# Performance work log

Measured on AMD Instinct MI355X. Metric: run time of the kernel, lower is better.

## Reference

```python
import jax, jax.numpy as jnp
import numpy as np

B, T, D, W, H = 64, 512, 768, 255, 8
DH = D // H

def layernorm(x, g, b, eps=1e-5):
    m = jnp.mean(x, axis=-1, keepdims=True)
    v = jnp.mean((x - m) ** 2, axis=-1, keepdims=True)
    return (x - m) * jax.lax.rsqrt(v + eps) * g + b

def setup_inputs() -> dict:
    key = jax.random.key(0)
    ks = list(jax.random.split(key, 12))
    p = lambda k, shape, s=0.02: (jax.random.normal(k, shape, jnp.float32) * s)
    # words_ids: -100 at CLS/SEP, each word spans 2 subtokens -> 255 words/row
    wi = np.full((B, T), -100, dtype=np.int32)
    pos = np.arange(1, T - 1)
    wi[:, 1:T - 1] = (pos - 1) // 2
    return {
        'output_bert': jax.random.normal(ks[0], (B, T, D), jnp.float32),
        'words_ids': jnp.asarray(wi),
        'Wq': p(ks[1], (D, D)), 'bq': jnp.zeros((D,), jnp.float32),
        'Wk': p(ks[2], (D, D)), 'bk': jnp.zeros((D,), jnp.float32),
        'Wv': p(ks[3], (D, D)), 'bv': jnp.zeros((D,), jnp.float32),
        'Wo': p(ks[4], (D, D)), 'bo': jnp.zeros((D,), jnp.float32),
        'ln1_g': jnp.ones((D,), jnp.float32), 'ln1_b': jnp.zeros((D,), jnp.float32),
        'W1f': p(ks[5], (D, 4 * D)), 'b1f': jnp.zeros((4 * D,), jnp.float32),
        'W2f': p(ks[6], (4 * D, D)), 'b2f': jnp.zeros((D,), jnp.float32),
        'ln2_g': jnp.ones((D,), jnp.float32), 'ln2_b': jnp.zeros((D,), jnp.float32),
        'ng': jnp.ones((D,), jnp.float32), 'nb': jnp.zeros((D,), jnp.float32),
        'lin_w': p(ks[7], (D, 2)), 'lin_b': jnp.zeros((2,), jnp.float32),
    }

def reference(output_bert, words_ids, Wq, bq, Wk, bk, Wv, bv, Wo, bo,
              ln1_g, ln1_b, W1f, b1f, W2f, b2f, ln2_g, ln2_b, ng, nb, lin_w, lin_b):
    Bsz = output_bert.shape[0]
    # --- first-subtoken gather: first token position of each word id ---
    hits = words_ids[:, None, :] == jnp.arange(W)[None, :, None]   # [B, W, T]
    first_idx = jnp.argmax(hits, axis=-1)                           # [B, W]
    feat = jnp.take_along_axis(output_bert, first_idx[..., None], axis=1)  # [B, W, D]
    # --- transformer encoder layer (post-norm, relu FFN) ---
    q = (feat @ Wq + bq).reshape(Bsz, W, H, DH)
    k = (feat @ Wk + bk).reshape(Bsz, W, H, DH)
    v = (feat @ Wv + bv).reshape(Bsz, W, H, DH)
    scores = jnp.einsum('bqhd,bkhd->bhqk', q, k) * (1.0 / np.sqrt(DH))
    attn = jax.nn.softmax(scores, axis=-1)
    ctx = jnp.einsum('bhqk,bkhd->bqhd', attn, v).reshape(Bsz, W, D)
    x = layernorm(feat + ctx @ Wo + bo, ln1_g, ln1_b)
    ff = jax.nn.relu(x @ W1f + b1f) @ W2f + b2f
    x = layernorm(x + ff, ln2_g, ln2_b)
    # --- final LayerNorm + Linear + softmax + argmax path ---
    x = layernorm(x, ng, nb)
    logits = x @ lin_w + lin_b
    ner_prob = jax.nn.softmax(logits, axis=-1)
    path = jnp.argmax(ner_prob, axis=-1)
    return ner_prob, path
```

## Files before the change

kernel.cpp:

```cpp
#include <hip/hip_runtime.h>
#include <cmath>

#define Bsz 64
#define Tt  512
#define Dd  768
#define Wn  255
#define Hh  8
#define DHd 96
#define NROWS (Bsz*Wn)

typedef _Float16 half_t;
typedef _Float16 f16x8 __attribute__((ext_vector_type(8)));
typedef _Float16 f16x4 __attribute__((ext_vector_type(4)));
typedef float f32x4 __attribute__((ext_vector_type(4)));

#define OFF_QKV_H 0
#define OFF_QKV_L 1769472
#define OFF_WO_H 3538944
#define OFF_WO_L 4128768
#define OFF_W1_H 4718592
#define OFF_W1_L 7077888
#define OFF_W2_H 9437184
#define OFF_W2_L 11796480
#define SLOTH 25165824
__device__ __align__(16) half_t g_w16[14155776];

__device__ __forceinline__ void gload16(const half_t* g, half_t* l) {
    __builtin_amdgcn_global_load_lds((const __attribute__((address_space(1))) void*)g,
                                     (__attribute__((address_space(3))) void*)l, 16, 0, 0);
}


__global__ void k_init_fi(int* fi) {
    int i = blockIdx.x * 256 + threadIdx.x;
    if (i < Bsz * Wn) fi[i] = 0x7fffffff;
}

__global__ void k_scan(const int* __restrict__ wid, int* __restrict__ fi) {
    int i = blockIdx.x * 256 + threadIdx.x;
    if (i >= Bsz * Tt) return;
    int b = i / Tt, t = i % Tt;
    int w = wid[i];
    if (w >= 0 && w < Wn) atomicMin(&fi[b * Wn + w], t);
}

__global__ void k_bcat(const float* __restrict__ bq, const float* __restrict__ bk,
                       const float* __restrict__ bv, float* __restrict__ o) {
    int i = blockIdx.x * 256 + threadIdx.x;
    if (i < 768) o[i] = bq[i];
    else if (i < 1536) o[i] = bk[i - 768];
    else if (i < 2304) o[i] = bv[i - 1536];
}

__global__ void k_gather(const float4* __restrict__ ob, const int* __restrict__ fi,
                         half_t* __restrict__ f16) {
    int i = blockIdx.x * 256 + threadIdx.x;
    if (i >= NROWS * 192) return;
    int r = i / 192, c = i % 192;
    int b = r / Wn;
    int idx = fi[r];
    if (idx == 0x7fffffff) idx = 0;
    float4 v = ob[((size_t)b * Tt + idx) * 192 + c];
    float a0 = v.x * 16.f, a1 = v.y * 16.f, a2 = v.z * 16.f, a3 = v.w * 16.f;
    half_t h0 = (half_t)a0, h1 = (half_t)a1, h2 = (half_t)a2, h3 = (half_t)a3;
    f16x4 hv = {h0, h1, h2, h3};
    f16x4 lv = {(half_t)(a0 - (float)h0), (half_t)(a1 - (float)h1),
                (half_t)(a2 - (float)h2), (half_t)(a3 - (float)h3)};
    size_t off = (size_t)r * 1536 + c * 4;
    *(f16x4*)&f16[off] = hv;
    *(f16x4*)&f16[off + 768] = lv;
}


__global__ void k_wsplit(const float* __restrict__ Wm, int K, int N,
                         size_t off_h, size_t off_l) {
    __shared__ float sm[32][33];
    const int tx = threadIdx.x, ty = threadIdx.y;
    const int n0 = blockIdx.x * 32, k0 = blockIdx.y * 32;
    #pragma unroll
    for (int r = 0; r < 4; ++r)
        sm[ty + r * 8][tx] = Wm[(size_t)(k0 + ty + r * 8) * N + n0 + tx];
    __syncthreads();
    half_t* oh = g_w16 + off_h;
    half_t* ol = g_w16 + off_l;
    #pragma unroll
    for (int r = 0; r < 4; ++r) {
        float v = 64.f * sm[tx][ty + r * 8];
        half_t hi = (half_t)v;
        size_t o = (size_t)(n0 + ty + r * 8) * K + k0 + tx;
        oh[o] = hi;
        ol[o] = (half_t)(v - (float)hi);
    }
}


template<int MODE, int AMODE, int NTILE>
__global__ __launch_bounds__(256, NTILE == 64 ? 3 : 2) void k_gemm16(
    const half_t* __restrict__ Ah, const half_t* __restrict__ Al, int lda,
    size_t boff_h, size_t boff_l,
    const float* __restrict__ bias,
    const void* __restrict__ res,
    void* __restrict__ out0, void* __restrict__ out1,
    int M, int N, int K) {
    constexpr int MI = (NTILE == 128 ? 4 : 2);
    __shared__ half_t sA[2][128 * 32];
    __shared__ half_t sB[2][NTILE * 32];
    const int tid = threadIdx.x;
    const int w = tid >> 6, l = tid & 63;
    int lin = blockIdx.y * gridDim.x + blockIdx.x;
    int rpx = gridDim.y >> 3;
    int j_ = lin >> 3;
    int jr = j_ / gridDim.x;
    int by = (lin & 7) * rpx + jr;
    int bx = j_ - jr * gridDim.x;
    const int row0 = by * 128, col0 = bx * NTILE;
    const half_t* Bh = g_w16 + boff_h;
    const half_t* Bl = g_w16 + boff_l;

    const int srow = l >> 2;
    const int skk  = (l & 3) * 8;
    const int fr = l & 15, qk = (l >> 4) * 8;
    const int mh = (NTILE == 128) ? (w >> 1) * 64 : w * 32;
    const int nh = (NTILE == 128) ? (w & 1) * 64 : 0;

    f32x4 acc[MI][4];
    #pragma unroll
    for (int i = 0; i < MI; ++i)
        #pragma unroll
        for (int j = 0; j < 4; ++j) acc[i][j] = (f32x4){0.f, 0.f, 0.f, 0.f};

    for (int k0 = 0; k0 < K; k0 += 32) {
        #pragma unroll
        for (int t = 0; t < 2; ++t) {
            int r = (w * 2 + t) * 16 + srow;
            int grA = row0 + r; if (grA >= M) grA = M - 1;
            half_t* da  = (half_t*)&sA[0][(w * 2 + t) * 512];
            half_t* da2 = (half_t*)&sA[1][(w * 2 + t) * 512];
            if (AMODE == 1) {
                int b = grA / 255, wl = grA - b * 255;
                int kk = k0 + skk;
                int h = kk / 96, d = kk - h * 96;
                size_t aoff = ((size_t)(b * 8 + h) * 256 + wl) * 192 + d;
                gload16(Ah + aoff, da);
                gload16(Al + aoff, da2);
            } else {
                gload16(Ah + (size_t)grA * lda + k0 + skk, da);
                gload16(Al + (size_t)grA * lda + k0 + skk, da2);
            }
            if (NTILE == 128 || t == 0) {
                int bs = (NTILE == 128) ? (w * 2 + t) : w;
                int grB = col0 + bs * 16 + srow;
                gload16(Bh + (size_t)grB * K + k0 + skk, (half_t*)&sB[0][bs * 512]);
                gload16(Bl + (size_t)grB * K + k0 + skk, (half_t*)&sB[1][bs * 512]);
            }
        }
        __syncthreads();
        f16x8 a0[MI], a1[MI], b0[4], b1[4];
        #pragma unroll
        for (int i = 0; i < MI; ++i) {
            a0[i] = *(const f16x8*)&sA[0][(mh + i * 16 + fr) * 32 + qk];
            a1[i] = *(const f16x8*)&sA[1][(mh + i * 16 + fr) * 32 + qk];
        }
        #pragma unroll
        for (int j = 0; j < 4; ++j) {
            b0[j] = *(const f16x8*)&sB[0][(nh + j * 16 + fr) * 32 + qk];
            b1[j] = *(const f16x8*)&sB[1][(nh + j * 16 + fr) * 32 + qk];
        }
        #pragma unroll
        for (int i = 0; i < MI; ++i)
            #pragma unroll
            for (int j = 0; j < 4; ++j) {
                acc[i][j] = __builtin_amdgcn_mfma_f32_16x16x32_f16(a0[i], b0[j], acc[i][j], 0, 0, 0);
                acc[i][j] = __builtin_amdgcn_mfma_f32_16x16x32_f16(a0[i], b1[j], acc[i][j], 0, 0, 0);
                acc[i][j] = __builtin_amdgcn_mfma_f32_16x16x32_f16(a1[i], b0[j], acc[i][j], 0, 0, 0);
            }
        __syncthreads();
    }

    const float dsc = 1.0f / 1024.0f;
    #pragma unroll
    for (int i = 0; i < MI; ++i) {
        #pragma unroll
        for (int r = 0; r < 4; ++r) {
            int row = row0 + mh + i * 16 + ((l >> 4) << 2) + r;
            if (row >= M) continue;
            #pragma unroll
            for (int j = 0; j < 4; ++j) {
                int col = col0 + nh + j * 16 + (l & 15);
                float vv = acc[i][j][r] * dsc + bias[col];
                if (MODE == 5) {
                    int b = row / 255, wl = row - b * 255;
                    int part = col / 768;
                    int cc = col - part * 768;
                    int h = cc / 96, d = cc - h * 96;
                    float t16 = vv * 16.f;
                    half_t hi = (half_t)t16;
                    half_t lo = (half_t)(t16 - (float)hi);
                    half_t* dst = (half_t*)out0 + (size_t)part * SLOTH;
                    size_t o = ((size_t)(b * 8 + h) * 256 + wl) * 192 + d;
                    dst[o] = hi; dst[o + 96] = lo;
                } else if (MODE == 1) {
                    const half_t* rp = (const half_t*)res;
                    vv += ((float)rp[(size_t)row * 1536 + col] +
                           (float)rp[(size_t)row * 1536 + 768 + col]) * 0.0625f;
                    ((float*)out0)[(size_t)row * N + col] = vv;
                } else if (MODE == 2) {
                    vv = fmaxf(vv, 0.f);
                    float t16 = vv * 16.f;
                    half_t hi = (half_t)t16;
                    ((half_t*)out0)[(size_t)row * N + col] = hi;
                    ((half_t*)out1)[(size_t)row * N + col] = (half_t)(t16 - (float)hi);
                } else {
                    vv += ((const float*)res)[(size_t)row * N + col];
                    ((float*)out0)[(size_t)row * N + col] = vv;
                }
            }
        }
    }
}


__global__ __launch_bounds__(256, 2) void k_attn2(half_t* __restrict__ qc,
                                                  const half_t* __restrict__ kk16,
                                                  const half_t* __restrict__ vv16) {
    __shared__ half_t sK[64][200];
    __shared__ half_t sVT[192][72];
    __shared__ float  sP[4][16][68];
    const int tid = threadIdx.x;
    const int w = tid >> 6, l = tid & 63;
    const int lr = l & 15, lc = l >> 4;
    const size_t base = (size_t)blockIdx.x * 49152;
    const float ssc = 0.10206207261596575f / 256.0f;

    for (int pass = 0; pass < 2; ++pass) {
        f32x4 O[2][6];
        float mrow[2][4], lrow[2][4];
        #pragma unroll
        for (int qs = 0; qs < 2; ++qs) {
            #pragma unroll
            for (int dn = 0; dn < 6; ++dn) O[qs][dn] = (f32x4){0.f, 0.f, 0.f, 0.f};
            #pragma unroll
            for (int r = 0; r < 4; ++r) { mrow[qs][r] = -3e38f; lrow[qs][r] = 0.f; }
        }
        for (int kt = 0; kt < 4; ++kt) {
            __syncthreads();
            #pragma unroll
            for (int c = 0; c < 6; ++c) {
                int ch = w + c * 4;
                *(f16x8*)&sK[l][ch * 8] =
                    *(const f16x8*)(kk16 + base + (size_t)(kt * 64 + l) * 192 + ch * 8);
            }
            #pragma unroll
            for (int c = 0; c < 6; ++c) {
                int ch = w + c * 4;
                f16x8 vv = *(const f16x8*)(vv16 + base + (size_t)(kt * 64 + l) * 192 + ch * 8);
                #pragma unroll
                for (int j = 0; j < 8; ++j) sVT[ch * 8 + j][l] = vv[j];
            }
            __syncthreads();
            #pragma unroll
            for (int qs = 0; qs < 2; ++qs) {
                const int qrow0 = (pass * 2 + qs) * 64 + w * 16;
                f16x8 qf0[3], qf1[3];
                #pragma unroll
                for (int s = 0; s < 3; ++s) {
                    qf0[s] = *(const f16x8*)(qc + base + (size_t)(qrow0 + lr) * 192 + s * 32 + lc * 8);
                    qf1[s] = *(const f16x8*)(qc + base + (size_t)(qrow0 + lr) * 192 + 96 + s * 32 + lc * 8);
                }
                f32x4 sacc[4];
                #pragma unroll
                for (int nt = 0; nt < 4; ++nt) sacc[nt] = (f32x4){0.f, 0.f, 0.f, 0.f};
                #pragma unroll
                for (int s = 0; s < 3; ++s)
                    #pragma unroll
                    for (int nt = 0; nt < 4; ++nt) {
                        f16x8 kh = *(const f16x8*)&sK[nt * 16 + lr][s * 32 + lc * 8];
                        f16x8 klo = *(const f16x8*)&sK[nt * 16 + lr][96 + s * 32 + lc * 8];
                        sacc[nt] = __builtin_amdgcn_mfma_f32_16x16x32_f16(qf0[s], kh, sacc[nt], 0, 0, 0);
                        sacc[nt] = __builtin_amdgcn_mfma_f32_16x16x32_f16(qf0[s], klo, sacc[nt], 0, 0, 0);
                        sacc[nt] = __builtin_amdgcn_mfma_f32_16x16x32_f16(qf1[s], kh, sacc[nt], 0, 0, 0);
                    }
                float sv[4][4], mx[4] = {-3e38f, -3e38f, -3e38f, -3e38f};
                #pragma unroll
                for (int nt = 0; nt < 4; ++nt) {
                    int key = kt * 64 + nt * 16 + lr;
                    #pragma unroll
                    for (int r = 0; r < 4; ++r) {
                        float s_ = sacc[nt][r] * ssc;
                        if (key >= 255) s_ = -3e38f;
                        sv[nt][r] = s_;
                        mx[r] = fmaxf(mx[r], s_);
                    }
                }
                #pragma unroll
                for (int r = 0; r < 4; ++r) {
                    mx[r] = fmaxf(mx[r], __shfl_xor(mx[r], 1));
                    mx[r] = fmaxf(mx[r], __shfl_xor(mx[r], 2));
                    mx[r] = fmaxf(mx[r], __shfl_xor(mx[r], 4));
                    mx[r] = fmaxf(mx[r], __shfl_xor(mx[r], 8));
                }
                float alpha[4], rsum[4];
                #pragma unroll
                for (int r = 0; r < 4; ++r) {
                    float mn = fmaxf(mrow[qs][r], mx[r]);
                    alpha[r] = __expf(mrow[qs][r] - mn);
                    mrow[qs][r] = mn;
                    rsum[r] = 0.f;
                }
                float pv[4][4];
                #pragma unroll
                for (int nt = 0; nt < 4; ++nt)
                    #pragma unroll
                    for (int r = 0; r < 4; ++r) {
                        float p = __expf(sv[nt][r] - mrow[qs][r]);
                        pv[nt][r] = p;
                        rsum[r] += p;
                    }
                #pragma unroll
                for (int r = 0; r < 4; ++r) {
                    rsum[r] += __shfl_xor(rsum[r], 1);
                    rsum[r] += __shfl_xor(rsum[r], 2);
                    rsum[r] += __shfl_xor(rsum[r], 4);
                    rsum[r] += __shfl_xor(rsum[r], 8);
                    lrow[qs][r] = lrow[qs][r] * alpha[r] + rsum[r];
                }
                #pragma unroll
                for (int dn = 0; dn < 6; ++dn)
                    #pragma unroll
                    for (int r = 0; r < 4; ++r) O[qs][dn][r] *= alpha[r];
                #pragma unroll
                for (int nt = 0; nt < 4; ++nt)
                    #pragma unroll
                    for (int r = 0; r < 4; ++r)
                        sP[w][lc * 4 + r][nt * 16 + lr] = pv[nt][r];
                #pragma unroll
                for (int ks = 0; ks < 2; ++ks) {
                    const float* pp = &sP[w][lr][ks * 32 + lc * 8];
                    f16x8 ph, pl;
                    #pragma unroll
                    for (int j = 0; j < 8; ++j) {
                        float p = pp[j];
                        half_t h_ = (half_t)p;
                        ph[j] = h_;
                        pl[j] = (half_t)(p - (float)h_);
                    }
                    #pragma unroll
                    for (int dn = 0; dn < 6; ++dn) {
                        f16x8 vh = *(const f16x8*)&sVT[dn * 16 + lr][ks * 32 + lc * 8];
                        f16x8 vl = *(const f16x8*)&sVT[96 + dn * 16 + lr][ks * 32 + lc * 8];
                        O[qs][dn] = __builtin_amdgcn_mfma_f32_16x16x32_f16(ph, vh, O[qs][dn], 0, 0, 0);
                        O[qs][dn] = __builtin_amdgcn_mfma_f32_16x16x32_f16(ph, vl, O[qs][dn], 0, 0, 0);
                        O[qs][dn] = __builtin_amdgcn_mfma_f32_16x16x32_f16(pl, vh, O[qs][dn], 0, 0, 0);
                    }
                }
            }
        }
        #pragma unroll
        for (int qs = 0; qs < 2; ++qs) {
            const int qrow0 = (pass * 2 + qs) * 64 + w * 16;
            #pragma unroll
            for (int r = 0; r < 4; ++r) {
                int qrow = qrow0 + lc * 4 + r;
                if (qrow >= Wn) continue;
                float inv = 1.0f / lrow[qs][r];
                #pragma unroll
                for (int dn = 0; dn < 6; ++dn) {
                    float val = O[qs][dn][r] * inv;
                    half_t hi = (half_t)val;
                    half_t lo = (half_t)(val - (float)hi);
                    size_t o = base + (size_t)qrow * 192 + dn * 16 + lr;
                    qc[o] = hi;
                    qc[o + 96] = lo;
                }
            }
        }
    }
}


__global__ __launch_bounds__(256) void k_ln1(const float* __restrict__ X, const float* __restrict__ g,
                                             const float* __restrict__ bt, float* __restrict__ Y,
                                             half_t* __restrict__ Y16) {
    const int r = blockIdx.x, tid = threadIdx.x;
    __shared__ float red[256];
    const float* x = X + (size_t)r * Dd;
    float x0 = x[tid], x1 = x[tid + 256], x2 = x[tid + 512];
    red[tid] = x0 + x1 + x2; __syncthreads();
    for (int s = 128; s > 0; s >>= 1) { if (tid < s) red[tid] += red[tid + s]; __syncthreads(); }
    float mean = red[0] * (1.0f / 768.0f);
    __syncthreads();
    float d0 = x0 - mean, d1 = x1 - mean, d2 = x2 - mean;
    red[tid] = d0 * d0 + d1 * d1 + d2 * d2; __syncthreads();
    for (int s = 128; s > 0; s >>= 1) { if (tid < s) red[tid] += red[tid + s]; __syncthreads(); }
    float rs = rsqrtf(red[0] * (1.0f / 768.0f) + 1e-5f);
    float* y = Y + (size_t)r * Dd;
    float y0 = d0 * rs * g[tid]       + bt[tid];
    float y1 = d1 * rs * g[tid + 256] + bt[tid + 256];
    float y2 = d2 * rs * g[tid + 512] + bt[tid + 512];
    y[tid] = y0; y[tid + 256] = y1; y[tid + 512] = y2;
    half_t* h = Y16 + (size_t)r * 1536;
    float t0 = y0 * 16.f, t1 = y1 * 16.f, t2 = y2 * 16.f;
    half_t h0 = (half_t)t0, h1 = (half_t)t1, h2 = (half_t)t2;
    h[tid] = h0; h[tid + 256] = h1; h[tid + 512] = h2;
    h[768 + tid] = (half_t)(t0 - (float)h0);
    h[768 + tid + 256] = (half_t)(t1 - (float)h1);
    h[768 + tid + 512] = (half_t)(t2 - (float)h2);
}


__global__ __launch_bounds__(256) void k_final2(const float* __restrict__ X,
                                                const float* __restrict__ g2, const float* __restrict__ b2,
                                                const float* __restrict__ ng, const float* __restrict__ nb,
                                                const float* __restrict__ lw, const float* __restrict__ lb,
                                                float* __restrict__ out) {
    const int r = blockIdx.x, tid = threadIdx.x;
    __shared__ float red[256];
    const float* x = X + (size_t)r * Dd;
    float x0 = x[tid], x1 = x[tid + 256], x2 = x[tid + 512];
    red[tid] = x0 + x1 + x2; __syncthreads();
    for (int s = 128; s > 0; s >>= 1) { if (tid < s) red[tid] += red[tid + s]; __syncthreads(); }
    float mean = red[0] * (1.0f / 768.0f);
    __syncthreads();
    float d0 = x0 - mean, d1 = x1 - mean, d2 = x2 - mean;
    red[tid] = d0 * d0 + d1 * d1 + d2 * d2; __syncthreads();
    for (int s = 128; s > 0; s >>= 1) { if (tid < s) red[tid] += red[tid + s]; __syncthreads(); }
    float rs = rsqrtf(red[0] * (1.0f / 768.0f) + 1e-5f);
    __syncthreads();
    float y0 = d0 * rs * g2[tid]       + b2[tid];
    float y1 = d1 * rs * g2[tid + 256] + b2[tid + 256];
    float y2 = d2 * rs * g2[tid + 512] + b2[tid + 512];
    red[tid] = y0 + y1 + y2; __syncthreads();
    for (int s = 128; s > 0; s >>= 1) { if (tid < s) red[tid] += red[tid + s]; __syncthreads(); }
    mean = red[0] * (1.0f / 768.0f);
    __syncthreads();
    float e0 = y0 - mean, e1 = y1 - mean, e2 = y2 - mean;
    red[tid] = e0 * e0 + e1 * e1 + e2 * e2; __syncthreads();
    for (int s = 128; s > 0; s >>= 1) { if (tid < s) red[tid] += red[tid + s]; __syncthreads(); }
    rs = rsqrtf(red[0] * (1.0f / 768.0f) + 1e-5f);
    __syncthreads();
    float n0 = e0 * rs * ng[tid]       + nb[tid];
    float n1 = e1 * rs * ng[tid + 256] + nb[tid + 256];
    float n2 = e2 * rs * ng[tid + 512] + nb[tid + 512];
    float l0 = n0 * lw[2 * tid]     + n1 * lw[2 * (tid + 256)]     + n2 * lw[2 * (tid + 512)];
    float l1 = n0 * lw[2 * tid + 1] + n1 * lw[2 * (tid + 256) + 1] + n2 * lw[2 * (tid + 512) + 1];
    red[tid] = l0; __syncthreads();
    for (int s = 128; s > 0; s >>= 1) { if (tid < s) red[tid] += red[tid + s]; __syncthreads(); }
    l0 = red[0]; __syncthreads();
    red[tid] = l1; __syncthreads();
    for (int s = 128; s > 0; s >>= 1) { if (tid < s) red[tid] += red[tid + s]; __syncthreads(); }
    l1 = red[0];
    if (tid == 0) {
        l0 += lb[0]; l1 += lb[1];
        float m = fmaxf(l0, l1);
        float e0_ = expf(l0 - m), e1_ = expf(l1 - m);
        float inv = 1.0f / (e0_ + e1_);
        out[2 * r] = e0_ * inv;
        out[2 * r + 1] = e1_ * inv;
        out[2 * NROWS + r] = (l1 > l0) ? 1.0f : 0.0f;
    }
}


extern "C" void kernel_launch(void* const* d_in, const int* in_sizes, int n_in,
                              void* d_out, int out_size, void* d_ws, size_t ws_size,
                              hipStream_t stream) {
    const float* ob  = (const float*)d_in[0];
    const int*   wid = (const int*)d_in[1];
    const float* Wq  = (const float*)d_in[2];  const float* bq  = (const float*)d_in[3];
    const float* Wk  = (const float*)d_in[4];  const float* bk  = (const float*)d_in[5];
    const float* Wv  = (const float*)d_in[6];  const float* bv  = (const float*)d_in[7];
    const float* Wo  = (const float*)d_in[8];  const float* bo  = (const float*)d_in[9];
    const float* g1  = (const float*)d_in[10]; const float* b1  = (const float*)d_in[11];
    const float* W1f = (const float*)d_in[12]; const float* b1f = (const float*)d_in[13];
    const float* W2f = (const float*)d_in[14]; const float* b2f = (const float*)d_in[15];
    const float* g2  = (const float*)d_in[16]; const float* b2  = (const float*)d_in[17];
    const float* ng  = (const float*)d_in[18]; const float* nb  = (const float*)d_in[19];
    const float* lw  = (const float*)d_in[20]; const float* lb  = (const float*)d_in[21];
    float* out = (float*)d_out;

    char* ws = (char*)d_ws;
    const size_t MB = 1u << 20;
    const size_t SLOT = 48 * MB;
    int* fi = (int*)ws;
    float* bcat = (float*)(ws + 262144);
    char* S1 = ws + MB;
    char* S2 = S1 + SLOT;
    char* S3 = S2 + SLOT;
    char* S4 = S3 + SLOT;

    half_t* feat16 = (half_t*)S1;
    half_t* q16    = (half_t*)S2;
    half_t* k16    = (half_t*)S3;
    half_t* v16    = (half_t*)S4;
    float*  t1     = (float*)S3;
    float*  xbuf   = (float*)S4;
    half_t* x16    = (half_t*)S2;
    half_t* ffh_h  = (half_t*)S1;
    half_t* ffh_l  = (half_t*)S3;
    float*  t2     = (float*)S2;

    k_wsplit<<<dim3(24, 24), dim3(32, 8), 0, stream>>>(Wq, 768, 768, 0, 1769472);
    k_wsplit<<<dim3(24, 24), dim3(32, 8), 0, stream>>>(Wk, 768, 768, 589824, 2359296);
    k_wsplit<<<dim3(24, 24), dim3(32, 8), 0, stream>>>(Wv, 768, 768, 1179648, 2949120);
    k_wsplit<<<dim3(24, 24), dim3(32, 8), 0, stream>>>(Wo, 768, 768, OFF_WO_H, OFF_WO_L);
    k_wsplit<<<dim3(96, 24), dim3(32, 8), 0, stream>>>(W1f, 768, 3072, OFF_W1_H, OFF_W1_L);
    k_wsplit<<<dim3(24, 96), dim3(32, 8), 0, stream>>>(W2f, 3072, 768, OFF_W2_H, OFF_W2_L);
    k_bcat<<<9, 256, 0, stream>>>(bq, bk, bv, bcat);

    k_init_fi<<<(Bsz * Wn + 255) / 256, 256, 0, stream>>>(fi);
    k_scan<<<(Bsz * Tt) / 256, 256, 0, stream>>>(wid, fi);
    k_gather<<<(NROWS * 192 + 255) / 256, 256, 0, stream>>>((const float4*)ob, fi, feat16);

    k_gemm16<5, 0, 128><<<dim3(18, 128), 256, 0, stream>>>(
        feat16, feat16 + 768, 1536, OFF_QKV_H, OFF_QKV_L,
        bcat, nullptr, q16, nullptr, NROWS, 2304, Dd);

    k_attn2<<<Bsz * Hh, 256, 0, stream>>>(q16, k16, v16);

    k_gemm16<1, 1, 128><<<dim3(6, 128), 256, 0, stream>>>(
        q16, q16 + 96, 0, OFF_WO_H, OFF_WO_L,
        bo, feat16, t1, nullptr, NROWS, Dd, Dd);
    k_ln1<<<NROWS, 256, 0, stream>>>(t1, g1, b1, xbuf, x16);

    for (int c = 0; c < 2; ++c) {
        const int r0 = c * 8160, mc = 8160;
        k_gemm16<2, 0, 128><<<dim3(24, 64), 256, 0, stream>>>(
            x16 + (size_t)r0 * 1536, x16 + (size_t)r0 * 1536 + 768, 1536,
            OFF_W1_H, OFF_W1_L, b1f, nullptr, ffh_h, ffh_l, mc, 3072, Dd);
        k_gemm16<3, 0, 64><<<dim3(12, 64), 256, 0, stream>>>(
            ffh_h, ffh_l, 3072, OFF_W2_H, OFF_W2_L, b2f, xbuf + (size_t)r0 * Dd,
            t2 + (size_t)r0 * Dd, nullptr, mc, Dd, 3072);
    }

    k_final2<<<NROWS, 256, 0, stream>>>(t2, g2, b2, ng, nb, lw, lb, out);
}
```

Before: 1.256 ms.

## Split attention blocks across query quarters with smaller key tiles for occupancy

The attention kernel now launches one block per (batch, head, 64-query chunk) instead of one block per (batch, head) looping over two passes. Key tiles shrink from 64 to 32 keys, which cuts shared memory and allows four blocks per CU. This raises parallelism and occupancy, at the cost of reloading K and V once per query chunk.

New measurement: 1.314 ms. 4.6% more time.

```diff
diff --git a/kernel.cpp b/kernel.cpp
--- a/kernel.cpp
+++ b/kernel.cpp
@@ -220,159 +220,148 @@
 }
 
 
-__global__ __launch_bounds__(256, 2) void k_attn2(half_t* __restrict__ qc,
+__global__ __launch_bounds__(256, 4) void k_attn3(half_t* __restrict__ qc,
                                                   const half_t* __restrict__ kk16,
                                                   const half_t* __restrict__ vv16) {
-    __shared__ half_t sK[64][200];
-    __shared__ half_t sVT[192][72];
-    __shared__ float  sP[4][16][68];
+    __shared__ half_t sK[32][200];
+    __shared__ half_t sVT[192][40];
+    __shared__ float  sP[4][16][36];
     const int tid = threadIdx.x;
     const int w = tid >> 6, l = tid & 63;
     const int lr = l & 15, lc = l >> 4;
-    const size_t base = (size_t)blockIdx.x * 49152;
+    const int bh = blockIdx.x >> 2, qq = blockIdx.x & 3;
+    const size_t base = (size_t)bh * 49152;
     const float ssc = 0.10206207261596575f / 256.0f;
-
-    for (int pass = 0; pass < 2; ++pass) {
-        f32x4 O[2][6];
-        float mrow[2][4], lrow[2][4];
-        #pragma unroll
-        for (int qs = 0; qs < 2; ++qs) {
-            #pragma unroll
-            for (int dn = 0; dn < 6; ++dn) O[qs][dn] = (f32x4){0.f, 0.f, 0.f, 0.f};
-            #pragma unroll
-            for (int r = 0; r < 4; ++r) { mrow[qs][r] = -3e38f; lrow[qs][r] = 0.f; }
-        }
-        for (int kt = 0; kt < 4; ++kt) {
-            __syncthreads();
-            #pragma unroll
-            for (int c = 0; c < 6; ++c) {
-                int ch = w + c * 4;
-                *(f16x8*)&sK[l][ch * 8] =
-                    *(const f16x8*)(kk16 + base + (size_t)(kt * 64 + l) * 192 + ch * 8);
-            }
-            #pragma unroll
-            for (int c = 0; c < 6; ++c) {
-                int ch = w + c * 4;
-                f16x8 vv = *(const f16x8*)(vv16 + base + (size_t)(kt * 64 + l) * 192 + ch * 8);
-                #pragma unroll
-                for (int j = 0; j < 8; ++j) sVT[ch * 8 + j][l] = vv[j];
-            }
-            __syncthreads();
-            #pragma unroll
-            for (int qs = 0; qs < 2; ++qs) {
-                const int qrow0 = (pass * 2 + qs) * 64 + w * 16;
-                f16x8 qf0[3], qf1[3];
-                #pragma unroll
-                for (int s = 0; s < 3; ++s) {
-                    qf0[s] = *(const f16x8*)(qc + base + (size_t)(qrow0 + lr) * 192 + s * 32 + lc * 8);
-                    qf1[s] = *(const f16x8*)(qc + base + (size_t)(qrow0 + lr) * 192 + 96 + s * 32 + lc * 8);
-                }
-                f32x4 sacc[4];
-                #pragma unroll
-                for (int nt = 0; nt < 4; ++nt) sacc[nt] = (f32x4){0.f, 0.f, 0.f, 0.f};
-                #pragma unroll
-                for (int s = 0; s < 3; ++s)
-                    #pragma unroll
-                    for (int nt = 0; nt < 4; ++nt) {
-                        f16x8 kh = *(const f16x8*)&sK[nt * 16 + lr][s * 32 + lc * 8];
-                        f16x8 klo = *(const f16x8*)&sK[nt * 16 + lr][96 + s * 32 + lc * 8];
-                        sacc[nt] = __builtin_amdgcn_mfma_f32_16x16x32_f16(qf0[s], kh, sacc[nt], 0, 0, 0);
-                        sacc[nt] = __builtin_amdgcn_mfma_f32_16x16x32_f16(qf0[s], klo, sacc[nt], 0, 0, 0);
-                        sacc[nt] = __builtin_amdgcn_mfma_f32_16x16x32_f16(qf1[s], kh, sacc[nt], 0, 0, 0);
-                    }
-                float sv[4][4], mx[4] = {-3e38f, -3e38f, -3e38f, -3e38f};
-                #pragma unroll
-                for (int nt = 0; nt < 4; ++nt) {
-                    int key = kt * 64 + nt * 16 + lr;
-                    #pragma unroll
-                    for (int r = 0; r < 4; ++r) {
-                        float s_ = sacc[nt][r] * ssc;
-                        if (key >= 255) s_ = -3e38f;
-                        sv[nt][r] = s_;
-                        mx[r] = fmaxf(mx[r], s_);
-                    }
-                }
-                #pragma unroll
-                for (int r = 0; r < 4; ++r) {
-                    mx[r] = fmaxf(mx[r], __shfl_xor(mx[r], 1));
-                    mx[r] = fmaxf(mx[r], __shfl_xor(mx[r], 2));
-                    mx[r] = fmaxf(mx[r], __shfl_xor(mx[r], 4));
-                    mx[r] = fmaxf(mx[r], __shfl_xor(mx[r], 8));
-                }
-                float alpha[4], rsum[4];
-                #pragma unroll
-                for (int r = 0; r < 4; ++r) {
-                    float mn = fmaxf(mrow[qs][r], mx[r]);
-                    alpha[r] = __expf(mrow[qs][r] - mn);
-                    mrow[qs][r] = mn;
-                    rsum[r] = 0.f;
-                }
-                float pv[4][4];
-                #pragma unroll
-                for (int nt = 0; nt < 4; ++nt)
-                    #pragma unroll
-                    for (int r = 0; r < 4; ++r) {
-                        float p = __expf(sv[nt][r] - mrow[qs][r]);
-                        pv[nt][r] = p;
-                        rsum[r] += p;
-                    }
-                #pragma unroll
-                for (int r = 0; r < 4; ++r) {
-                    rsum[r] += __shfl_xor(rsum[r], 1);
-                    rsum[r] += __shfl_xor(rsum[r], 2);
-                    rsum[r] += __shfl_xor(rsum[r], 4);
-                    rsum[r] += __shfl_xor(rsum[r], 8);
-                    lrow[qs][r] = lrow[qs][r] * alpha[r] + rsum[r];
-                }
-                #pragma unroll
-                for (int dn = 0; dn < 6; ++dn)
-                    #pragma unroll
-                    for (int r = 0; r < 4; ++r) O[qs][dn][r] *= alpha[r];
-                #pragma unroll
-                for (int nt = 0; nt < 4; ++nt)
-                    #pragma unroll
-                    for (int r = 0; r < 4; ++r)
-                        sP[w][lc * 4 + r][nt * 16 + lr] = pv[nt][r];
-                #pragma unroll
-                for (int ks = 0; ks < 2; ++ks) {
-                    const float* pp = &sP[w][lr][ks * 32 + lc * 8];
-                    f16x8 ph, pl;
-                    #pragma unroll
-                    for (int j = 0; j < 8; ++j) {
-                        float p = pp[j];
-                        half_t h_ = (half_t)p;
-                        ph[j] = h_;
-                        pl[j] = (half_t)(p - (float)h_);
-                    }
-                    #pragma unroll
-                    for (int dn = 0; dn < 6; ++dn) {
-                        f16x8 vh = *(const f16x8*)&sVT[dn * 16 + lr][ks * 32 + lc * 8];
-                        f16x8 vl = *(const f16x8*)&sVT[96 + dn * 16 + lr][ks * 32 + lc * 8];
-                        O[qs][dn] = __builtin_amdgcn_mfma_f32_16x16x32_f16(ph, vh, O[qs][dn], 0, 0, 0);
-                        O[qs][dn] = __builtin_amdgcn_mfma_f32_16x16x32_f16(ph, vl, O[qs][dn], 0, 0, 0);
-                        O[qs][dn] = __builtin_amdgcn_mfma_f32_16x16x32_f16(pl, vh, O[qs][dn], 0, 0, 0);
-                    }
-                }
-            }
-        }
-        #pragma unroll
-        for (int qs = 0; qs < 2; ++qs) {
-            const int qrow0 = (pass * 2 + qs) * 64 + w * 16;
+    const int qrow0 = qq * 64 + w * 16;
+
+    f16x8 qf0[3], qf1[3];
+    #pragma unroll
+    for (int s = 0; s < 3; ++s) {
+        qf0[s] = *(const f16x8*)(qc + base + (size_t)(qrow0 + lr) * 192 + s * 32 + lc * 8);
+        qf1[s] = *(const f16x8*)(qc + base + (size_t)(qrow0 + lr) * 192 + 96 + s * 32 + lc * 8);
+    }
+    f32x4 O[6];
+    #pragma unroll
+    for (int dn = 0; dn < 6; ++dn) O[dn] = (f32x4){0.f, 0.f, 0.f, 0.f};
+    float mrow[4] = {-3e38f, -3e38f, -3e38f, -3e38f};
+    float lrow[4] = {0.f, 0.f, 0.f, 0.f};
+
+    for (int kt = 0; kt < 8; ++kt) {
+        __syncthreads();
+        #pragma unroll
+        for (int c = 0; c < 3; ++c) {
+            int u = c * 256 + tid;
+            int key = u / 24, ch = u % 24;
+            *(f16x8*)&sK[key][ch * 8] =
+                *(const f16x8*)(kk16 + base + (size_t)(kt * 32 + key) * 192 + ch * 8);
+        }
+        #pragma unroll
+        for (int c = 0; c < 12; ++c) {
+            int ch = (l >> 5) * 12 + c;
+            f16x8 vv = *(const f16x8*)(vv16 + base + (size_t)(kt * 32 + (l & 31)) * 192 + ch * 8);
+            #pragma unroll
+            for (int j = 0; j < 8; ++j) sVT[ch * 8 + j][l & 31] = vv[j];
+        }
+        __syncthreads();
+        f32x4 sacc[2];
+        #pragma unroll
+        for (int nt = 0; nt < 2; ++nt) sacc[nt] = (f32x4){0.f, 0.f, 0.f, 0.f};
+        #pragma unroll
+        for (int s = 0; s < 3; ++s)
+            #pragma unroll
+            for (int nt = 0; nt < 2; ++nt) {
+                f16x8 kh = *(const f16x8*)&sK[nt * 16 + lr][s * 32 + lc * 8];
+                f16x8 klo = *(const f16x8*)&sK[nt * 16 + lr][96 + s * 32 + lc * 8];
+                sacc[nt] = __builtin_amdgcn_mfma_f32_16x16x32_f16(qf0[s], kh, sacc[nt], 0, 0, 0);
+                sacc[nt] = __builtin_amdgcn_mfma_f32_16x16x32_f16(qf0[s], klo, sacc[nt], 0, 0, 0);
+                sacc[nt] = __builtin_amdgcn_mfma_f32_16x16x32_f16(qf1[s], kh, sacc[nt], 0, 0, 0);
+            }
+        float sv[2][4], mx[4] = {-3e38f, -3e38f, -3e38f, -3e38f};
+        #pragma unroll
+        for (int nt = 0; nt < 2; ++nt) {
+            int key = kt * 32 + nt * 16 + lr;
             #pragma unroll
             for (int r = 0; r < 4; ++r) {
-                int qrow = qrow0 + lc * 4 + r;
-                if (qrow >= Wn) continue;
-                float inv = 1.0f / lrow[qs][r];
-                #pragma unroll
-                for (int dn = 0; dn < 6; ++dn) {
-                    float val = O[qs][dn][r] * inv;
-                    half_t hi = (half_t)val;
-                    half_t lo = (half_t)(val - (float)hi);
-                    size_t o = base + (size_t)qrow * 192 + dn * 16 + lr;
-                    qc[o] = hi;
-                    qc[o + 96] = lo;
-                }
-            }
+                float s_ = sacc[nt][r] * ssc;
+                if (key >= 255) s_ = -3e38f;
+                sv[nt][r] = s_;
+                mx[r] = fmaxf(mx[r], s_);
+            }
+        }
+        #pragma unroll
+        for (int r = 0; r < 4; ++r) {
+            mx[r] = fmaxf(mx[r], __shfl_xor(mx[r], 1));
+            mx[r] = fmaxf(mx[r], __shfl_xor(mx[r], 2));
+            mx[r] = fmaxf(mx[r], __shfl_xor(mx[r], 4));
+            mx[r] = fmaxf(mx[r], __shfl_xor(mx[r], 8));
+        }
+        float alpha[4], rsum[4];
+        #pragma unroll
+        for (int r = 0; r < 4; ++r) {
+            float mn = fmaxf(mrow[r], mx[r]);
+            alpha[r] = __expf(mrow[r] - mn);
+            mrow[r] = mn;
+            rsum[r] = 0.f;
+        }
+        float pv[2][4];
+        #pragma unroll
+        for (int nt = 0; nt < 2; ++nt)
+            #pragma unroll
+            for (int r = 0; r < 4; ++r) {
+                float p = __expf(sv[nt][r] - mrow[r]);
+                pv[nt][r] = p;
+                rsum[r] += p;
+            }
+        #pragma unroll
+        for (int r = 0; r < 4; ++r) {
+            rsum[r] += __shfl_xor(rsum[r], 1);
+            rsum[r] += __shfl_xor(rsum[r], 2);
+            rsum[r] += __shfl_xor(rsum[r], 4);
+            rsum[r] += __shfl_xor(rsum[r], 8);
+            lrow[r] = lrow[r] * alpha[r] + rsum[r];
+        }
+        #pragma unroll
+        for (int dn = 0; dn < 6; ++dn)
+            #pragma unroll
+            for (int r = 0; r < 4; ++r) O[dn][r] *= alpha[r];
+        #pragma unroll
+        for (int nt = 0; nt < 2; ++nt)
+            #pragma unroll
+            for (int r = 0; r < 4; ++r)
+                sP[w][lc * 4 + r][nt * 16 + lr] = pv[nt][r];
+        {
+            const float* pp = &sP[w][lr][lc * 8];
+            f16x8 ph, pl;
+            #pragma unroll
+            for (int j = 0; j < 8; ++j) {
+                float p = pp[j];
+                half_t h_ = (half_t)p;
+                ph[j] = h_;
+                pl[j] = (half_t)(p - (float)h_);
+            }
+            #pragma unroll
+            for (int dn = 0; dn < 6; ++dn) {
+                f16x8 vh = *(const f16x8*)&sVT[dn * 16 + lr][lc * 8];
+                f16x8 vl = *(const f16x8*)&sVT[96 + dn * 16 + lr][lc * 8];
+                O[dn] = __builtin_amdgcn_mfma_f32_16x16x32_f16(ph, vh, O[dn], 0, 0, 0);
+                O[dn] = __builtin_amdgcn_mfma_f32_16x16x32_f16(ph, vl, O[dn], 0, 0, 0);
+                O[dn] = __builtin_amdgcn_mfma_f32_16x16x32_f16(pl, vh, O[dn], 0, 0, 0);
+            }
+        }
+    }
+    #pragma unroll
+    for (int r = 0; r < 4; ++r) {
+        int qrow = qrow0 + lc * 4 + r;
+        if (qrow >= Wn) continue;
+        float inv = 1.0f / lrow[r];
+        #pragma unroll
+        for (int dn = 0; dn < 6; ++dn) {
+            float val = O[dn][r] * inv;
+            half_t hi = (half_t)val;
+            half_t lo = (half_t)(val - (float)hi);
+            size_t o = base + (size_t)qrow * 192 + dn * 16 + lr;
+            qc[o] = hi;
+            qc[o + 96] = lo;
         }
     }
 }
@@ -515,7 +504,7 @@
         feat16, feat16 + 768, 1536, OFF_QKV_H, OFF_QKV_L,
         bcat, nullptr, q16, nullptr, NROWS, 2304, Dd);
 
-    k_attn2<<<Bsz * Hh, 256, 0, stream>>>(q16, k16, v16);
+    k_attn3<<<Bsz * Hh * 4, 256, 0, stream>>>(q16, k16, v16);
 
     k_gemm16<1, 1, 128><<<dim3(6, 128), 256, 0, stream>>>(
         q16, q16 + 96, 0, OFF_WO_H, OFF_WO_L,
```
